# Optimization experiments

Hardware: AMD Instinct MI355X
Metric: run time of the kernel (lower is better)

Reference implementation:

```python
import jax, jax.numpy as jnp
import numpy as np

N_NODES = 100000
N_EDGES = 3200000
D = 8


def setup_inputs() -> dict:
    key = jax.random.key(0)
    k1, k2, k3 = jax.random.split(key, 3)
    x = jax.random.normal(k1, (N_NODES, D), dtype=jnp.float32)
    edge_index = jax.random.randint(k2, (2, N_EDGES), 0, N_NODES, dtype=jnp.int64)
    # distances-like positive edge attrs in [0.5, 1.5) to avoid divide blow-up
    edge_attr = jax.random.uniform(k3, (N_EDGES, D), dtype=jnp.float32,
                                   minval=0.5, maxval=1.5)
    return {"x": x, "edge_index": edge_index, "edge_attr": edge_attr}


def reference(x, edge_index, edge_attr):
    # EdgeSpatialDerivative: (dest - src) / edge_attr
    src = x[edge_index[0]]            # [E, D] gather
    dest = x[edge_index[1]]           # [E, D] gather
    edge_deriv = (dest - src) / edge_attr

    # NodeSpatialDerivative: scatter_mean(edge_deriv, edge_index[1], dim=0)
    seg = edge_index[1]
    sums = jax.ops.segment_sum(edge_deriv, seg, num_segments=N_NODES)
    counts = jax.ops.segment_sum(jnp.ones((edge_deriv.shape[0],), dtype=edge_deriv.dtype),
                                 seg, num_segments=N_NODES)
    node_deriv = sums / jnp.maximum(counts, 1.0)[:, None]  # empty segments -> 0

    # MetaLayer returns (x_updated, edge_attr_updated, u)
    return node_deriv, edge_deriv
```

## Files before the change

### kernel.cpp

```cpp
#include <hip/hip_runtime.h>
#include <math.h>

#define D 8
#define NPC 512
#define NPCSH 9
#define NCMAX 512
#define EPB 3072
#define APT 1024
#define BCH 1536
#define BPT 1024
#define BSH 6
#define BMASK 63
#define NBMAX 1600
#define EPBF 6250
#define RPT5 512

__device__ __forceinline__ unsigned pk_bf16(float a, float b) {
    unsigned ua = __float_as_uint(a), ub = __float_as_uint(b);
    ua = (ua + 0x7FFFu + ((ua >> 16) & 1u)) >> 16;
    ub = (ub + 0x7FFFu + ((ub >> 16) & 1u)) >> 16;
    return ua | (ub << 16);
}
__device__ __forceinline__ float bf_lo(unsigned u) { return __uint_as_float(u << 16); }
__device__ __forceinline__ float bf_hi(unsigned u) { return __uint_as_float(u & 0xFFFF0000u); }

__global__ void zero_cursors_kernel(unsigned* __restrict__ cur, int n) {
    int i = blockIdx.x * blockDim.x + threadIdx.x;
    if (i < n) cur[i] = 0u;
}

template<int NB>
__device__ __forceinline__ void scan_bins(unsigned* hist, unsigned* incl,
                                          unsigned* starts, unsigned* cur,
                                          unsigned* wsum, unsigned* woff) {
    int tid = threadIdx.x;
    if (tid < NB) {
        int l = tid & 63;
        unsigned v = hist[tid], s = v;
#pragma unroll
        for (int dd = 1; dd < 64; dd <<= 1) {
            unsigned tt = __shfl_up(s, dd, 64);
            if (l >= dd) s += tt;
        }
        incl[tid] = s;
        if (l == 63) wsum[tid >> 6] = s;
    }
    __syncthreads();
    if (tid == 0) {
        unsigned o = 0;
#pragma unroll
        for (int w = 0; w < NB / 64; ++w) { woff[w] = o; o += wsum[w]; }
    }
    __syncthreads();
    if (tid < NB) {
        unsigned st = incl[tid] - hist[tid] + woff[tid >> 6];
        starts[tid] = st;
        cur[tid] = st;
    }
    __syncthreads();
}


__global__ __launch_bounds__(APT) void edge_sort2_kernel(
    const float4* __restrict__ x4,
    const int* __restrict__ src_idx,
    const int* __restrict__ dst_idx,
    const float4* __restrict__ ea4,
    float4* __restrict__ out_edge4,
    unsigned* __restrict__ gcur,
    uint4* __restrict__ vals,
    unsigned short* __restrict__ locs,
    int n_edges, int nc, int cap)
{
    __shared__ uint4 pay[EPB];
    __shared__ unsigned key[EPB];
    __shared__ unsigned short sidx[EPB];
    __shared__ unsigned hist[NCMAX];
    __shared__ unsigned incl[NCMAX];
    __shared__ unsigned starts[NCMAX];
    __shared__ unsigned cur[NCMAX];
    __shared__ unsigned base[NCMAX];
    __shared__ unsigned wsum[NCMAX / 64], woff[NCMAX / 64];

    for (int c = threadIdx.x; c < NCMAX; c += APT) hist[c] = 0u;
    __syncthreads();

    const int start = blockIdx.x * EPB;
    int lim = n_edges - start;
    if (lim > EPB) lim = EPB;
    if (lim < 0) lim = 0;

    for (int i = threadIdx.x; i < lim; i += APT) {
        int e = start + i;
        int s = src_idx[e];
        int t = dst_idx[e];
        float4 xs0 = x4[(size_t)s * 2 + 0];
        float4 xs1 = x4[(size_t)s * 2 + 1];
        float4 xd0 = x4[(size_t)t * 2 + 0];
        float4 xd1 = x4[(size_t)t * 2 + 1];
        float4 a0  = ea4[(size_t)e * 2 + 0];
        float4 a1  = ea4[(size_t)e * 2 + 1];
        float4 d0, d1;
        d0.x = (xd0.x - xs0.x) / a0.x;
        d0.y = (xd0.y - xs0.y) / a0.y;
        d0.z = (xd0.z - xs0.z) / a0.z;
        d0.w = (xd0.w - xs0.w) / a0.w;
        d1.x = (xd1.x - xs1.x) / a1.x;
        d1.y = (xd1.y - xs1.y) / a1.y;
        d1.z = (xd1.z - xs1.z) / a1.z;
        d1.w = (xd1.w - xs1.w) / a1.w;
        out_edge4[(size_t)e * 2 + 0] = d0;
        out_edge4[(size_t)e * 2 + 1] = d1;
        uint4 v = { pk_bf16(d0.x, d0.y), pk_bf16(d0.z, d0.w),
                    pk_bf16(d1.x, d1.y), pk_bf16(d1.z, d1.w) };
        pay[i] = v;
        key[i] = (unsigned)t;
        atomicAdd(&hist[(unsigned)t >> NPCSH], 1u);
    }
    __syncthreads();

    scan_bins<NCMAX>(hist, incl, starts, cur, wsum, woff);

    if (threadIdx.x < (unsigned)nc)
        base[threadIdx.x] = hist[threadIdx.x]
            ? atomicAdd(&gcur[threadIdx.x], hist[threadIdx.x]) : 0u;
    __syncthreads();

    for (int i = threadIdx.x; i < lim; i += APT) {
        unsigned c = key[i] >> NPCSH;
        unsigned p = atomicAdd(&cur[c], 1u);
        sidx[p] = (unsigned short)i;
    }
    __syncthreads();

    for (int p = threadIdx.x; p < lim; p += APT) {
        unsigned i   = sidx[p];
        unsigned t   = key[i];
        unsigned c   = t >> NPCSH;
        unsigned addr = base[c] + ((unsigned)p - starts[c]);
        if (addr < (unsigned)cap) {
            size_t gi = (size_t)c * cap + addr;
            vals[gi] = pay[i];
            locs[gi] = (unsigned short)(t & (NPC - 1));
        }
    }
}


__global__ __launch_bounds__(BPT) void coarse_reduce_kernel(
    const unsigned* __restrict__ gcur,
    const uint4* __restrict__ vals,
    const unsigned short* __restrict__ locs,
    float4* __restrict__ out_node4,
    int n_nodes, int cap)
{
    __shared__ float acc[NPC * 9];
    __shared__ uint4 vstage[BCH];
    __shared__ unsigned hist[NPC];
    __shared__ unsigned incl[NPC];
    __shared__ unsigned starts[NPC];
    __shared__ unsigned cur[NPC];
    __shared__ unsigned wsum[NPC / 64], woff[NPC / 64];

    const int c = blockIdx.x;
    int count = (int)gcur[c];
    if (count > cap) count = cap;
    const uint4* vsrc = vals + (size_t)c * cap;
    const unsigned short* lsrc = locs + (size_t)c * cap;

    for (int j = threadIdx.x; j < NPC * 9; j += BPT) acc[j] = 0.0f;
    __syncthreads();

    for (int cb = 0; cb < count; cb += BCH) {
        int cnt = count - cb;
        if (cnt > BCH) cnt = BCH;

        for (int j = threadIdx.x; j < NPC; j += BPT) hist[j] = 0u;
        __syncthreads();

        uint4 r0, r1;
        unsigned l0 = 0xFFFFu, l1 = 0xFFFFu;
        int i0 = threadIdx.x, i1 = threadIdx.x + BPT;
        if (i0 < cnt) { r0 = vsrc[cb + i0]; l0 = lsrc[cb + i0]; atomicAdd(&hist[l0], 1u); }
        if (i1 < cnt) { r1 = vsrc[cb + i1]; l1 = lsrc[cb + i1]; atomicAdd(&hist[l1], 1u); }
        __syncthreads();

        scan_bins<NPC>(hist, incl, starts, cur, wsum, woff);

        if (l0 != 0xFFFFu) { unsigned p = atomicAdd(&cur[l0], 1u); vstage[p] = r0; }
        if (l1 != 0xFFFFu) { unsigned p = atomicAdd(&cur[l1], 1u); vstage[p] = r1; }
        __syncthreads();

        if (threadIdx.x < NPC) {
            unsigned s = starts[threadIdx.x];
            unsigned e = (threadIdx.x == NPC - 1) ? (unsigned)cnt
                                                  : starts[threadIdx.x + 1];
            if (e > s) {
                float f0 = 0.f, f1 = 0.f, f2 = 0.f, f3 = 0.f;
                float f4 = 0.f, f5 = 0.f, f6 = 0.f, f7 = 0.f;
                for (unsigned j = s; j < e; ++j) {
                    uint4 v = vstage[j];
                    f0 += bf_lo(v.x); f1 += bf_hi(v.x);
                    f2 += bf_lo(v.y); f3 += bf_hi(v.y);
                    f4 += bf_lo(v.z); f5 += bf_hi(v.z);
                    f6 += bf_lo(v.w); f7 += bf_hi(v.w);
                }
                float* a = acc + threadIdx.x * 9;
                a[0] += f0; a[1] += f1; a[2] += f2; a[3] += f3;
                a[4] += f4; a[5] += f5; a[6] += f6; a[7] += f7;
                a[8] += (float)(e - s);
            }
        }
        __syncthreads();
    }

    if (threadIdx.x < NPC) {
        int node = (c << NPCSH) + threadIdx.x;
        if (node < n_nodes) {
            const float* a = acc + threadIdx.x * 9;
            float inv = 1.0f / fmaxf(a[8], 1.0f);
            float4 o0 = { a[0] * inv, a[1] * inv, a[2] * inv, a[3] * inv };
            float4 o1 = { a[4] * inv, a[5] * inv, a[6] * inv, a[7] * inv };
            out_node4[(size_t)node * 2 + 0] = o0;
            out_node4[(size_t)node * 2 + 1] = o1;
        }
    }
}


__global__ __launch_bounds__(APT) void edge_phase_kernel(
    const float4* __restrict__ x4,
    const int* __restrict__ src_idx,
    const int* __restrict__ dst_idx,
    const float4* __restrict__ ea4,
    float4* __restrict__ out_edge4,
    unsigned* __restrict__ cursors,
    unsigned* __restrict__ pairs,
    int n_edges, int nb, int cap)
{
    __shared__ unsigned hist[NBMAX];
    __shared__ unsigned base[NBMAX];
    __shared__ unsigned cur[NBMAX];
    __shared__ unsigned tld[EPBF];

    for (int b = threadIdx.x; b < nb; b += APT) { hist[b] = 0u; cur[b] = 0u; }
    __syncthreads();

    const int start = blockIdx.x * EPBF;
    int lim = n_edges - start;
    if (lim > EPBF) lim = EPBF;
    if (lim < 0) lim = 0;

    for (int i = threadIdx.x; i < lim; i += APT) {
        int e = start + i;
        int s = src_idx[e];
        int t = dst_idx[e];
        tld[i] = (unsigned)t;
        float4 xs0 = x4[(size_t)s * 2 + 0];
        float4 xs1 = x4[(size_t)s * 2 + 1];
        float4 xd0 = x4[(size_t)t * 2 + 0];
        float4 xd1 = x4[(size_t)t * 2 + 1];
        float4 a0  = ea4[(size_t)e * 2 + 0];
        float4 a1  = ea4[(size_t)e * 2 + 1];
        float4 d0, d1;
        d0.x = (xd0.x - xs0.x) / a0.x;
        d0.y = (xd0.y - xs0.y) / a0.y;
        d0.z = (xd0.z - xs0.z) / a0.z;
        d0.w = (xd0.w - xs0.w) / a0.w;
        d1.x = (xd1.x - xs1.x) / a1.x;
        d1.y = (xd1.y - xs1.y) / a1.y;
        d1.z = (xd1.z - xs1.z) / a1.z;
        d1.w = (xd1.w - xs1.w) / a1.w;
        out_edge4[(size_t)e * 2 + 0] = d0;
        out_edge4[(size_t)e * 2 + 1] = d1;
        atomicAdd(&hist[t >> BSH], 1u);
    }
    __syncthreads();

    for (int b = threadIdx.x; b < nb; b += APT)
        base[b] = hist[b] ? atomicAdd(&cursors[b], hist[b]) : 0u;
    __syncthreads();

    for (int i = threadIdx.x; i < lim; i += APT) {
        int e = start + i;
        unsigned t = tld[i];
        unsigned b = t >> BSH;
        unsigned p = base[b] + atomicAdd(&cur[b], 1u);
        if (p < (unsigned)cap)
            pairs[(size_t)b * cap + p] = ((unsigned)e << BSH) | (t & BMASK);
    }
}

__device__ __forceinline__ void acc9(float* __restrict__ acc, unsigned loc,
                                     float4 d0, float4 d1) {
    float* a = acc + loc * 9;
    atomicAdd(a + 0, d0.x);
    atomicAdd(a + 1, d0.y);
    atomicAdd(a + 2, d0.z);
    atomicAdd(a + 3, d0.w);
    atomicAdd(a + 4, d1.x);
    atomicAdd(a + 5, d1.y);
    atomicAdd(a + 6, d1.z);
    atomicAdd(a + 7, d1.w);
    atomicAdd(a + 8, 1.0f);
}

__global__ __launch_bounds__(RPT5) void bucket_reduce_kernel(
    const unsigned* __restrict__ cursors,
    const unsigned* __restrict__ pairs,
    const float4* __restrict__ edge4,
    float4* __restrict__ out_node4,
    int n_nodes, int cap)
{
    __shared__ float acc[64 * 9];
    for (int j = threadIdx.x; j < 64 * 9; j += RPT5) acc[j] = 0.0f;
    __syncthreads();

    const int b = blockIdx.x;
    int count = (int)cursors[b];
    if (count > cap) count = cap;
    const unsigned* pb = pairs + (size_t)b * cap;

    for (int i = threadIdx.x; i < count; i += RPT5) {
        unsigned pr = pb[i];
        float4 d0 = edge4[(size_t)(pr >> BSH) * 2 + 0];
        float4 d1 = edge4[(size_t)(pr >> BSH) * 2 + 1];
        acc9(acc, pr & BMASK, d0, d1);
    }
    __syncthreads();

    if (threadIdx.x < 128) {
        int loc  = threadIdx.x >> 1;
        int half = threadIdx.x & 1;
        int node = (b << BSH) + loc;
        if (node < n_nodes) {
            const float* a = acc + loc * 9;
            float inv = 1.0f / fmaxf(a[8], 1.0f);
            float4 o = { a[half * 4 + 0] * inv, a[half * 4 + 1] * inv,
                         a[half * 4 + 2] * inv, a[half * 4 + 3] * inv };
            out_node4[(size_t)node * 2 + half] = o;
        }
    }
}


__global__ void fb_zero_kernel(float* __restrict__ node_out, int n_node_f,
                               float* __restrict__ counts, int n_counts) {
    int stride = gridDim.x * blockDim.x;
    int tid = blockIdx.x * blockDim.x + threadIdx.x;
    for (int i = tid; i < n_node_f; i += stride) node_out[i] = 0.0f;
    for (int i = tid; i < n_counts; i += stride) counts[i] = 0.0f;
}

__global__ void fb_edge_kernel(const float4* __restrict__ x4,
                               const int* __restrict__ src_idx,
                               const int* __restrict__ dst_idx,
                               const float4* __restrict__ ea4,
                               float4* __restrict__ out_edge4,
                               float* __restrict__ node_sums,
                               float* __restrict__ counts,
                               int n_edges) {
    int e = blockIdx.x * blockDim.x + threadIdx.x;
    if (e >= n_edges) return;
    int s = src_idx[e];
    int t = dst_idx[e];
    float4 xs0 = x4[(size_t)s * 2 + 0];
    float4 xs1 = x4[(size_t)s * 2 + 1];
    float4 xd0 = x4[(size_t)t * 2 + 0];
    float4 xd1 = x4[(size_t)t * 2 + 1];
    float4 a0  = ea4[(size_t)e * 2 + 0];
    float4 a1  = ea4[(size_t)e * 2 + 1];
    float4 d0, d1;
    d0.x = (xd0.x - xs0.x) / a0.x;
    d0.y = (xd0.y - xs0.y) / a0.y;
    d0.z = (xd0.z - xs0.z) / a0.z;
    d0.w = (xd0.w - xs0.w) / a0.w;
    d1.x = (xd1.x - xs1.x) / a1.x;
    d1.y = (xd1.y - xs1.y) / a1.y;
    d1.z = (xd1.z - xs1.z) / a1.z;
    d1.w = (xd1.w - xs1.w) / a1.w;
    out_edge4[(size_t)e * 2 + 0] = d0;
    out_edge4[(size_t)e * 2 + 1] = d1;
    float* sp = node_sums + (size_t)t * D;
    atomicAdd(sp + 0, d0.x);
    atomicAdd(sp + 1, d0.y);
    atomicAdd(sp + 2, d0.z);
    atomicAdd(sp + 3, d0.w);
    atomicAdd(sp + 4, d1.x);
    atomicAdd(sp + 5, d1.y);
    atomicAdd(sp + 6, d1.z);
    atomicAdd(sp + 7, d1.w);
    atomicAdd(counts + t, 1.0f);
}

__global__ void fb_node_kernel(float4* __restrict__ node4,
                               const float* __restrict__ counts,
                               int n_nodes) {
    int n = blockIdx.x * blockDim.x + threadIdx.x;
    if (n >= n_nodes) return;
    float inv = 1.0f / fmaxf(counts[n], 1.0f);
    float4 s0 = node4[(size_t)n * 2 + 0];
    float4 s1 = node4[(size_t)n * 2 + 1];
    s0.x *= inv; s0.y *= inv; s0.z *= inv; s0.w *= inv;
    s1.x *= inv; s1.y *= inv; s1.z *= inv; s1.w *= inv;
    node4[(size_t)n * 2 + 0] = s0;
    node4[(size_t)n * 2 + 1] = s1;
}


extern "C" void kernel_launch(void* const* d_in, const int* in_sizes, int n_in,
                              void* d_out, int out_size, void* d_ws, size_t ws_size,
                              hipStream_t stream) {
    const float* x  = (const float*)d_in[0];
    const int*   ei = (const int*)d_in[1];
    const float* ea = (const float*)d_in[2];

    const int n_nodes = in_sizes[0] / D;
    const int n_edges = in_sizes[2] / D;

    const int* src_idx = ei;
    const int* dst_idx = ei + n_edges;

    float* out_node = (float*)d_out;
    float* out_edge = out_node + (size_t)n_nodes * D;

    {
        const int nc = (n_nodes + NPC - 1) >> NPCSH;
        long long meanc = nc > 0 ? (long long)n_edges / nc : 0;
        int capc = (int)(meanc + meanc / 8 + 1024);
        size_t gcur_b = ((size_t)nc * 4 + 255) & ~(size_t)255;
        size_t vals_b = (size_t)nc * capc * 16;
        size_t locs_b = (size_t)nc * capc * 2;
        size_t need = gcur_b + vals_b + locs_b + 256;

        if (nc >= 1 && nc <= NCMAX && ws_size >= need) {
            unsigned*       gcur = (unsigned*)d_ws;
            uint4*          vals = (uint4*)((char*)d_ws + gcur_b);
            unsigned short* locs = (unsigned short*)((char*)d_ws + gcur_b + vals_b);

            int blocksA = (n_edges + EPB - 1) / EPB;
            zero_cursors_kernel<<<(nc + 255) / 256, 256, 0, stream>>>(gcur, nc);
            edge_sort2_kernel<<<blocksA, APT, 0, stream>>>(
                (const float4*)x, src_idx, dst_idx, (const float4*)ea,
                (float4*)out_edge, gcur, vals, locs, n_edges, nc, capc);
            coarse_reduce_kernel<<<nc, BPT, 0, stream>>>(
                gcur, vals, locs, (float4*)out_node, n_nodes, capc);
            return;
        }
    }

    {
        const int nb = (n_nodes + BMASK) >> BSH;
        int cap = (int)(((long long)n_edges / (nb > 0 ? nb : 1) + 256) * 3 / 2);
        cap = (cap + 3) & ~3;
        size_t cursors_bytes = ((size_t)nb * 4 + 255) & ~(size_t)255;
        size_t need = cursors_bytes + (size_t)nb * cap * 4;
        if (nb <= NBMAX && ws_size >= need) {
            unsigned* cursors = (unsigned*)d_ws;
            unsigned* pairs   = (unsigned*)((char*)d_ws + cursors_bytes);

            int blocksA = (n_edges + EPBF - 1) / EPBF;
            zero_cursors_kernel<<<(nb + 255) / 256, 256, 0, stream>>>(cursors, nb);
            edge_phase_kernel<<<blocksA, APT, 0, stream>>>(
                (const float4*)x, src_idx, dst_idx, (const float4*)ea,
                (float4*)out_edge, cursors, pairs, n_edges, nb, cap);
            bucket_reduce_kernel<<<nb, RPT5, 0, stream>>>(
                cursors, pairs, (const float4*)out_edge, (float4*)out_node,
                n_nodes, cap);
            return;
        }
    }

    {
        float* counts = (float*)d_ws;
        int n = n_nodes * D;
        int blocks = (n + 255) / 256;
        if (blocks > 2048) blocks = 2048;
        fb_zero_kernel<<<blocks, 256, 0, stream>>>(out_node, n, counts, n_nodes);
        fb_edge_kernel<<<(n_edges + 255) / 256, 256, 0, stream>>>(
            (const float4*)x, src_idx, dst_idx, (const float4*)ea,
            (float4*)out_edge, out_node, counts, n_edges);
        fb_node_kernel<<<(n_nodes + 255) / 256, 256, 0, stream>>>(
            (float4*)out_node, counts, n_nodes);
    }
}
```

Before: 167.5 us.

## Split edge compute from bucket sort into separate kernels

```diff
diff --git a/kernel.cpp b/kernel.cpp
--- a/kernel.cpp
+++ b/kernel.cpp
@@ -61,20 +61,48 @@
 }
 
 
-__global__ __launch_bounds__(APT) void edge_sort2_kernel(
+__global__ __launch_bounds__(256) void edge_compute_kernel(
     const float4* __restrict__ x4,
     const int* __restrict__ src_idx,
     const int* __restrict__ dst_idx,
     const float4* __restrict__ ea4,
     float4* __restrict__ out_edge4,
+    int n_edges)
+{
+    int e = blockIdx.x * 256 + threadIdx.x;
+    if (e >= n_edges) return;
+    int s = src_idx[e];
+    int t = dst_idx[e];
+    float4 xs0 = x4[(size_t)s * 2 + 0];
+    float4 xs1 = x4[(size_t)s * 2 + 1];
+    float4 xd0 = x4[(size_t)t * 2 + 0];
+    float4 xd1 = x4[(size_t)t * 2 + 1];
+    float4 a0  = ea4[(size_t)e * 2 + 0];
+    float4 a1  = ea4[(size_t)e * 2 + 1];
+    float4 d0, d1;
+    d0.x = (xd0.x - xs0.x) / a0.x;
+    d0.y = (xd0.y - xs0.y) / a0.y;
+    d0.z = (xd0.z - xs0.z) / a0.z;
+    d0.w = (xd0.w - xs0.w) / a0.w;
+    d1.x = (xd1.x - xs1.x) / a1.x;
+    d1.y = (xd1.y - xs1.y) / a1.y;
+    d1.z = (xd1.z - xs1.z) / a1.z;
+    d1.w = (xd1.w - xs1.w) / a1.w;
+    out_edge4[(size_t)e * 2 + 0] = d0;
+    out_edge4[(size_t)e * 2 + 1] = d1;
+}
+
+
+__global__ __launch_bounds__(APT) void edge_sortk_kernel(
+    const int* __restrict__ dst_idx,
+    const float4* __restrict__ edge4,
     unsigned* __restrict__ gcur,
     uint4* __restrict__ vals,
     unsigned short* __restrict__ locs,
     int n_edges, int nc, int cap)
 {
     __shared__ uint4 pay[EPB];
-    __shared__ unsigned key[EPB];
-    __shared__ unsigned short sidx[EPB];
+    __shared__ unsigned meta[EPB];
     __shared__ unsigned hist[NCMAX];
     __shared__ unsigned incl[NCMAX];
     __shared__ unsigned starts[NCMAX];
@@ -91,31 +119,8 @@
     if (lim < 0) lim = 0;
 
     for (int i = threadIdx.x; i < lim; i += APT) {
-        int e = start + i;
-        int s = src_idx[e];
-        int t = dst_idx[e];
-        float4 xs0 = x4[(size_t)s * 2 + 0];
-        float4 xs1 = x4[(size_t)s * 2 + 1];
-        float4 xd0 = x4[(size_t)t * 2 + 0];
-        float4 xd1 = x4[(size_t)t * 2 + 1];
-        float4 a0  = ea4[(size_t)e * 2 + 0];
-        float4 a1  = ea4[(size_t)e * 2 + 1];
-        float4 d0, d1;
-        d0.x = (xd0.x - xs0.x) / a0.x;
-        d0.y = (xd0.y - xs0.y) / a0.y;
-        d0.z = (xd0.z - xs0.z) / a0.z;
-        d0.w = (xd0.w - xs0.w) / a0.w;
-        d1.x = (xd1.x - xs1.x) / a1.x;
-        d1.y = (xd1.y - xs1.y) / a1.y;
-        d1.z = (xd1.z - xs1.z) / a1.z;
-        d1.w = (xd1.w - xs1.w) / a1.w;
-        out_edge4[(size_t)e * 2 + 0] = d0;
-        out_edge4[(size_t)e * 2 + 1] = d1;
-        uint4 v = { pk_bf16(d0.x, d0.y), pk_bf16(d0.z, d0.w),
-                    pk_bf16(d1.x, d1.y), pk_bf16(d1.z, d1.w) };
-        pay[i] = v;
-        key[i] = (unsigned)t;
-        atomicAdd(&hist[(unsigned)t >> NPCSH], 1u);
+        unsigned t = (unsigned)dst_idx[start + i];
+        atomicAdd(&hist[t >> NPCSH], 1u);
     }
     __syncthreads();
 
@@ -124,23 +129,27 @@
     if (threadIdx.x < (unsigned)nc)
         base[threadIdx.x] = hist[threadIdx.x]
             ? atomicAdd(&gcur[threadIdx.x], hist[threadIdx.x]) : 0u;
-    __syncthreads();
 
     for (int i = threadIdx.x; i < lim; i += APT) {
-        unsigned c = key[i] >> NPCSH;
-        unsigned p = atomicAdd(&cur[c], 1u);
-        sidx[p] = (unsigned short)i;
+        int e = start + i;
+        unsigned t = (unsigned)dst_idx[e];
+        float4 d0 = edge4[(size_t)e * 2 + 0];
+        float4 d1 = edge4[(size_t)e * 2 + 1];
+        unsigned p = atomicAdd(&cur[t >> NPCSH], 1u);
+        uint4 v = { pk_bf16(d0.x, d0.y), pk_bf16(d0.z, d0.w),
+                    pk_bf16(d1.x, d1.y), pk_bf16(d1.z, d1.w) };
+        pay[p] = v;
+        meta[p] = t;
     }
     __syncthreads();
 
     for (int p = threadIdx.x; p < lim; p += APT) {
-        unsigned i   = sidx[p];
-        unsigned t   = key[i];
-        unsigned c   = t >> NPCSH;
+        unsigned t = meta[p];
+        unsigned c = t >> NPCSH;
         unsigned addr = base[c] + ((unsigned)p - starts[c]);
         if (addr < (unsigned)cap) {
             size_t gi = (size_t)c * cap + addr;
-            vals[gi] = pay[i];
+            vals[gi] = pay[p];
             locs[gi] = (unsigned short)(t & (NPC - 1));
         }
     }
@@ -438,11 +447,14 @@
             uint4*          vals = (uint4*)((char*)d_ws + gcur_b);
             unsigned short* locs = (unsigned short*)((char*)d_ws + gcur_b + vals_b);
 
-            int blocksA = (n_edges + EPB - 1) / EPB;
             zero_cursors_kernel<<<(nc + 255) / 256, 256, 0, stream>>>(gcur, nc);
-            edge_sort2_kernel<<<blocksA, APT, 0, stream>>>(
+            edge_compute_kernel<<<(n_edges + 255) / 256, 256, 0, stream>>>(
                 (const float4*)x, src_idx, dst_idx, (const float4*)ea,
-                (float4*)out_edge, gcur, vals, locs, n_edges, nc, capc);
+                (float4*)out_edge, n_edges);
+            int blocksS = (n_edges + EPB - 1) / EPB;
+            edge_sortk_kernel<<<blocksS, APT, 0, stream>>>(
+                dst_idx, (const float4*)out_edge, gcur, vals, locs,
+                n_edges, nc, capc);
             coarse_reduce_kernel<<<nc, BPT, 0, stream>>>(
                 gcur, vals, locs, (float4*)out_node, n_nodes, capc);
             return;
```

Result: slower. 174.6 us (+4.2%).
